# Kernel tuning notes

Measured on AMD Instinct MI355X. Metric: run time of the kernel, lower is better.

Reference implementation:

```python
import jax, jax.numpy as jnp
import numpy as np

N_NODES = 100000
N_EDGES = 1600000
IN_CH = 128
HID = 128
EPS = 1e-5


def setup_inputs() -> dict:
    key = jax.random.key(0)
    ks = jax.random.split(key, 16)
    x = jax.random.normal(ks[0], (N_NODES, IN_CH), dtype=jnp.float32)
    edge_index = jax.random.randint(ks[1], (2, N_EDGES), 0, N_NODES, dtype=jnp.int64)
    dims = [(IN_CH, HID), (HID, HID), (HID, HID // 2)]
    params = {}
    for i, (di, do) in enumerate(dims):
        params[f'w{i}'] = jax.random.normal(ks[2 + i], (di, do), dtype=jnp.float32) * (1.0 / np.sqrt(di))
        params[f'b{i}'] = jnp.zeros((do,), dtype=jnp.float32)
        params[f'g{i}'] = jnp.ones((do,), dtype=jnp.float32)
        params[f'be{i}'] = jnp.zeros((do,), dtype=jnp.float32)
    params['wc1'] = jax.random.normal(ks[8], (HID // 2, 32), dtype=jnp.float32) * (1.0 / np.sqrt(HID // 2))
    params['bc1'] = jnp.zeros((32,), dtype=jnp.float32)
    params['wc2'] = jax.random.normal(ks[9], (32, 1), dtype=jnp.float32) * (1.0 / np.sqrt(32))
    params['bc2'] = jnp.zeros((1,), dtype=jnp.float32)
    return {'x': x, 'edge_index': edge_index, **params}


def _gcn_forward(x, edge_index, w0, b0, g0, be0, w1, b1, g1, be1, w2, b2, g2, be2, wc1, bc1, wc2, bc2):
    n = x.shape[0]
    # add self-loops (GCNConv default)
    loops = jnp.arange(n, dtype=edge_index.dtype)
    src = jnp.concatenate([edge_index[0], loops])  # [E+N]
    dst = jnp.concatenate([edge_index[1], loops])
    # symmetric normalization: deg over targets (incl. self loops)
    deg = jax.ops.segment_sum(jnp.ones_like(dst, dtype=x.dtype), dst, num_segments=n)
    dis = jax.lax.rsqrt(jnp.maximum(deg, 1e-12))  # deg>=1 due to self loops
    norm = (dis[src] * dis[dst])[:, None]  # [E+N, 1]

    def layer(h, w, b, g, be):
        h = h @ w                                   # [N, d_out]
        h = jax.ops.segment_sum(h[src] * norm, dst, num_segments=n) + b
        mu = jnp.mean(h, axis=0)
        var = jnp.mean(jnp.square(h - mu), axis=0)  # biased var (torch BN)
        h = (h - mu) * jax.lax.rsqrt(var + EPS) * g + be
        return jax.nn.relu(h)                       # dropout: identity (eval)

    h = layer(x, w0, b0, g0, be0)
    h = layer(h, w1, b1, g1, be1)
    h = layer(h, w2, b2, g2, be2)
    h = jax.nn.relu(h @ wc1 + bc1)
    return (h @ wc2 + bc2)[:, 0]  # [N]


def reference(x, edge_index, w0, b0, g0, be0, w1, b1, g1, be1, w2, b2, g2, be2, wc1, bc1, wc2, bc2):
    return _gcn_forward(x, edge_index, w0, b0, g0, be0, w1, b1, g1, be1, w2, b2, g2, be2, wc1, bc1, wc2, bc2)
```

## Files before the change

### kernel.cpp

```cpp
#include <hip/hip_runtime.h>


typedef __attribute__((ext_vector_type(8))) short short8;
typedef __attribute__((ext_vector_type(4))) float f32x4;

#define BIN_SHIFT 7
#define BIN_NODES 128
#define CAPB 4096
#define CAP 64

__device__ __forceinline__ float b2f(unsigned short u) {
    return __uint_as_float(((unsigned)u) << 16);
}
__device__ __forceinline__ unsigned short f2bf(float f) {
    unsigned u = __float_as_uint(f);
    return (unsigned short)((u + 0x7fff + ((u >> 16) & 1)) >> 16);
}

__global__ __launch_bounds__(256) void part1_kernel(const int* __restrict__ eidx,
                                                    int E, int nbins, int chunk,
                                                    int* __restrict__ bin_fill,
                                                    int* __restrict__ binned) {
    __shared__ int cntS[1024];
    __shared__ int baseS[1024];
    int tid = threadIdx.x;
    for (int b = tid; b < nbins; b += 256) cntS[b] = 0;
    __syncthreads();
    int e0 = blockIdx.x * chunk;
    int e1 = min(e0 + chunk, E);
    for (int e = e0 + tid; e < e1; e += 256)
        atomicAdd(&cntS[eidx[E + e] >> BIN_SHIFT], 1);
    __syncthreads();
    for (int b = tid; b < nbins; b += 256) {
        baseS[b] = atomicAdd(&bin_fill[b], cntS[b]);
        cntS[b] = 0;
    }
    __syncthreads();
    for (int e = e0 + tid; e < e1; e += 256) {
        int d = eidx[E + e];
        int s = eidx[e];
        int b = d >> BIN_SHIFT;
        int p = baseS[b] + atomicAdd(&cntS[b], 1);
        if (p < CAPB) binned[b * CAPB + p] = (s << BIN_SHIFT) | (d & (BIN_NODES - 1));
    }
}

__global__ __launch_bounds__(256) void part2_kernel(const int* __restrict__ bin_fill,
                                                    const int* __restrict__ binned,
                                                    int N, int* __restrict__ fill,
                                                    float* __restrict__ dis,
                                                    int* __restrict__ stage) {
    __shared__ int lfill[BIN_NODES];
    int b = blockIdx.x, tid = threadIdx.x;
    if (tid < BIN_NODES) lfill[tid] = 0;
    __syncthreads();
    int cnt = min(bin_fill[b], CAPB);
    const int* seg = binned + b * CAPB;
    for (int i = tid; i < cnt; i += 256) {
        int v = seg[i];
        int dl = v & (BIN_NODES - 1);
        int p = atomicAdd(&lfill[dl], 1);
        int node = (b << BIN_SHIFT) + dl;
        if (p < CAP) stage[(node << 6) + p] = v >> BIN_SHIFT;
    }
    __syncthreads();
    if (tid < BIN_NODES) {
        int node = (b << BIN_SHIFT) + tid;
        if (node < N) {
            int c = lfill[tid];
            fill[node] = c;
            dis[node] = rsqrtf((float)c + 1.0f);
        }
    }
}

__global__ void wfrag_kernel(const float* __restrict__ w,
                             unsigned short* __restrict__ wf, int total, int C) {
    int tid = blockIdx.x * 256 + threadIdx.x;
    if (tid >= total) return;
    int j = tid & 7;
    int lane = (tid >> 3) & 63;
    int q = (tid >> 9) & 3;
    int n_tile = tid >> 11;
    int k = q * 32 + (lane >> 4) * 8 + j;
    int n = n_tile * 16 + (lane & 15);
    wf[tid] = f2bf(w[k * C + n]);
}

__device__ __forceinline__ void load8(const float* p, float4& lo, float4& hi) {
    lo = *(const float4*)p;
    hi = *(const float4*)(p + 4);
}
__device__ __forceinline__ void load8(const unsigned short* p, float4& lo, float4& hi) {
    int4 q = *(const int4*)p;
    lo = make_float4(__uint_as_float((unsigned)q.x << 16),
                     __uint_as_float((unsigned)q.x & 0xffff0000u),
                     __uint_as_float((unsigned)q.y << 16),
                     __uint_as_float((unsigned)q.y & 0xffff0000u));
    hi = make_float4(__uint_as_float((unsigned)q.z << 16),
                     __uint_as_float((unsigned)q.z & 0xffff0000u),
                     __uint_as_float((unsigned)q.w << 16),
                     __uint_as_float((unsigned)q.w & 0xffff0000u));
}

template <int C, typename InT>
__global__ __launch_bounds__(256, 5) void mfma_gemm_kernel(
    const InT* __restrict__ xin, const unsigned short* __restrict__ wf,
    const float* __restrict__ scale, const float* __restrict__ shift,
    const float* __restrict__ dis, unsigned short* __restrict__ out, int N) {
    constexpr int NT = C / 16;
    constexpr int WFRAGS = NT * 4 * 64;
    __shared__ short8 ws[WFRAGS];
    int tid = threadIdx.x;
    for (int i = tid; i < WFRAGS; i += 256) ws[i] = ((const short8*)wf)[i];

    int lane = tid & 63;
    int wave = tid >> 6;
    int m0 = blockIdx.x * 64 + wave * 16;
    int r15 = lane & 15, r4 = lane >> 4;
    f32x4 acc[NT];
#pragma unroll
    for (int t = 0; t < NT; t++) acc[t] = (f32x4){0.f, 0.f, 0.f, 0.f};
    int row0 = m0 + r15;
    int row0c = min(row0, N - 1);
    __syncthreads();

#pragma unroll
    for (int q = 0; q < 4; q++) {
        int kb = q * 32 + r4 * 8;
        float4 a0l, a0h;
        load8(xin + (size_t)row0c * 128 + kb, a0l, a0h);
        if (scale) {
            float4 scl = *(const float4*)&scale[kb];
            float4 sch = *(const float4*)&scale[kb + 4];
            float4 shl = *(const float4*)&shift[kb];
            float4 shh = *(const float4*)&shift[kb + 4];
            a0l.x = fmaxf(a0l.x * scl.x + shl.x, 0.f);
            a0l.y = fmaxf(a0l.y * scl.y + shl.y, 0.f);
            a0l.z = fmaxf(a0l.z * scl.z + shl.z, 0.f);
            a0l.w = fmaxf(a0l.w * scl.w + shl.w, 0.f);
            a0h.x = fmaxf(a0h.x * sch.x + shh.x, 0.f);
            a0h.y = fmaxf(a0h.y * sch.y + shh.y, 0.f);
            a0h.z = fmaxf(a0h.z * sch.z + shh.z, 0.f);
            a0h.w = fmaxf(a0h.w * sch.w + shh.w, 0.f);
        }
        short8 a0;
        a0[0] = (short)f2bf(a0l.x); a0[1] = (short)f2bf(a0l.y);
        a0[2] = (short)f2bf(a0l.z); a0[3] = (short)f2bf(a0l.w);
        a0[4] = (short)f2bf(a0h.x); a0[5] = (short)f2bf(a0h.y);
        a0[6] = (short)f2bf(a0h.z); a0[7] = (short)f2bf(a0h.w);
#pragma unroll
        for (int nt = 0; nt < NT; nt++) {
            short8 b = ws[(nt * 4 + q) * 64 + lane];
            acc[nt] = __builtin_amdgcn_mfma_f32_16x16x32_bf16(a0, b, acc[nt], 0, 0, 0);
        }
    }
    float d0r[4];
#pragma unroll
    for (int r = 0; r < 4; r++) {
        int rowa = m0 + r4 * 4 + r;
        d0r[r] = (rowa < N) ? dis[rowa] : 0.f;
    }
#pragma unroll
    for (int nt = 0; nt < NT; nt++) {
        int col = nt * 16 + r15;
#pragma unroll
        for (int r = 0; r < 4; r++) {
            int rowa = m0 + r4 * 4 + r;
            if (rowa < N) out[(size_t)rowa * C + col] = f2bf(acc[nt][r] * d0r[r]);
        }
    }
}

__global__ __launch_bounds__(256) void agg128_kernel(
    const unsigned short* __restrict__ h, const int* __restrict__ fill,
    const int* __restrict__ stage, const float* __restrict__ dis,
    unsigned short* __restrict__ out, int N) {
    int lane = threadIdx.x & 63;
    int node = blockIdx.x * 4 + (threadIdx.x >> 6);
    if (node >= N) return;
    float dn = dis[node];
    ushort2 sv = ((const ushort2*)(h + (size_t)node * 128))[lane];
    float2 acc = make_float2(b2f(sv.x), b2f(sv.y));
    int ne = min(fill[node], CAP);
    int pk = (lane < ne) ? stage[(node << 6) + lane] : 0;
    int j = 0;
    for (; j + 16 <= ne; j += 16) {
        ushort2 a[16];
#pragma unroll
        for (int t = 0; t < 16; t++) {
            int s = __builtin_amdgcn_readlane(pk, j + t);
            a[t] = ((const ushort2*)(h + (size_t)s * 128))[lane];
        }
#pragma unroll
        for (int t = 0; t < 16; t++) { acc.x += b2f(a[t].x); acc.y += b2f(a[t].y); }
    }
    for (; j + 8 <= ne; j += 8) {
        ushort2 a[8];
#pragma unroll
        for (int t = 0; t < 8; t++) {
            int s = __builtin_amdgcn_readlane(pk, j + t);
            a[t] = ((const ushort2*)(h + (size_t)s * 128))[lane];
        }
#pragma unroll
        for (int t = 0; t < 8; t++) { acc.x += b2f(a[t].x); acc.y += b2f(a[t].y); }
    }
    for (; j + 4 <= ne; j += 4) {
        ushort2 a[4];
#pragma unroll
        for (int t = 0; t < 4; t++) {
            int s = __builtin_amdgcn_readlane(pk, j + t);
            a[t] = ((const ushort2*)(h + (size_t)s * 128))[lane];
        }
#pragma unroll
        for (int t = 0; t < 4; t++) { acc.x += b2f(a[t].x); acc.y += b2f(a[t].y); }
    }
    for (; j < ne; j++) {
        int s = __builtin_amdgcn_readlane(pk, j);
        ushort2 a = ((const ushort2*)(h + (size_t)s * 128))[lane];
        acc.x += b2f(a.x);
        acc.y += b2f(a.y);
    }
    ((ushort2*)(out + (size_t)node * 128))[lane] =
        make_ushort2(f2bf(acc.x * dn), f2bf(acc.y * dn));
}

__global__ __launch_bounds__(256) void agg64_kernel(
    const unsigned short* __restrict__ h, const int* __restrict__ fill,
    const int* __restrict__ stage, const float* __restrict__ dis,
    unsigned short* __restrict__ out, int N) {
    int lane = threadIdx.x & 63;
    int node = blockIdx.x * 4 + (threadIdx.x >> 6);
    if (node >= N) return;
    int half = lane >> 5, ch = lane & 31;
    float dn = dis[node];
    float2 acc = make_float2(0.f, 0.f);
    if (half == 0) {
        ushort2 sv = ((const ushort2*)(h + (size_t)node * 64))[ch];
        acc.x = b2f(sv.x);
        acc.y = b2f(sv.y);
    }
    int ne = min(fill[node], CAP);
    int pk = (lane < ne) ? stage[(node << 6) + lane] : 0;
    int j = 0;
    for (; j + 16 <= ne; j += 16) {
        ushort2 a[8];
#pragma unroll
        for (int t = 0; t < 8; t++) {
            int s = __shfl(pk, j + 2 * t + half);
            a[t] = ((const ushort2*)(h + (size_t)s * 64))[ch];
        }
#pragma unroll
        for (int t = 0; t < 8; t++) { acc.x += b2f(a[t].x); acc.y += b2f(a[t].y); }
    }
    for (; j + 8 <= ne; j += 8) {
        ushort2 a[4];
#pragma unroll
        for (int t = 0; t < 4; t++) {
            int s = __shfl(pk, j + 2 * t + half);
            a[t] = ((const ushort2*)(h + (size_t)s * 64))[ch];
        }
#pragma unroll
        for (int t = 0; t < 4; t++) { acc.x += b2f(a[t].x); acc.y += b2f(a[t].y); }
    }
    for (; j < ne; j += 2) {
        int jj = j + half;
        int s = __shfl(pk, jj);
        bool v = jj < ne;
        ushort2 a = ((const ushort2*)(h + (size_t)s * 64))[ch];
        acc.x += v ? b2f(a.x) : 0.f;
        acc.y += v ? b2f(a.y) : 0.f;
    }
    acc.x += __shfl_down(acc.x, 32);
    acc.y += __shfl_down(acc.y, 32);
    if (half == 0)
        ((ushort2*)(out + (size_t)node * 64))[ch] =
            make_ushort2(f2bf(acc.x * dn), f2bf(acc.y * dn));
}

template <int C>
__global__ __launch_bounds__(256) void stats_kernel(const unsigned short* __restrict__ h,
                                                    int N, float* __restrict__ sums) {
    constexpr int R = 256 / C;
    int c = threadIdx.x % C;
    int rg = threadIdx.x / C;
    float s = 0.f, s2 = 0.f;
    for (int n = blockIdx.x * R + rg; n < N; n += gridDim.x * R) {
        float v = b2f(h[(size_t)n * C + c]);
        s += v;
        s2 += v * v;
    }
    __shared__ float red[256], red2[256];
    red[threadIdx.x] = s;
    red2[threadIdx.x] = s2;
    __syncthreads();
    if (rg == 0) {
#pragma unroll
        for (int r = 1; r < R; r++) {
            s += red[r * C + c];
            s2 += red2[r * C + c];
        }
        atomicAdd(&sums[c], s);
        atomicAdd(&sums[C + c], s2);
    }
}

template <int C>
__global__ void finalize_kernel(const float* __restrict__ sums,
                                const float* __restrict__ g,
                                const float* __restrict__ be, int N,
                                float* __restrict__ scale, float* __restrict__ shift) {
    int c = threadIdx.x;
    float inv_n = 1.0f / (float)N;
    float mean = sums[c] * inv_n;
    float var = sums[C + c] * inv_n - mean * mean;
    var = var > 0.f ? var : 0.f;
    float sc = g[c] * rsqrtf(var + 1e-5f);
    scale[c] = sc;
    shift[c] = be[c] - mean * sc;
}

__global__ __launch_bounds__(256) void head_kernel(
    const unsigned short* __restrict__ h, const float* __restrict__ scale,
    const float* __restrict__ shift, const float* __restrict__ wc1,
    const float* __restrict__ bc1, const float* __restrict__ wc2,
    const float* __restrict__ bc2, float* __restrict__ out, int N) {
    __shared__ float w1s[64 * 32];
    __shared__ float b1s[32], w2s[32], s2s[64], sh2[64];
    __shared__ float b2s;
    int tid = threadIdx.x;
    for (int i = tid; i < 64 * 32; i += 256) w1s[i] = wc1[i];
    if (tid < 32) { b1s[tid] = bc1[tid]; w2s[tid] = wc2[tid]; }
    if (tid < 64) { s2s[tid] = scale[tid]; sh2[tid] = shift[tid]; }
    if (tid == 0) b2s = bc2[0];
    __syncthreads();
    int n = blockIdx.x * 256 + tid;
    if (n >= N) return;
    float v[64];
#pragma unroll
    for (int k = 0; k < 64; k++) {
        float x = b2f(h[(size_t)n * 64 + k]) * s2s[k] + sh2[k];
        v[k] = x > 0.f ? x : 0.f;
    }
    float o = b2s;
#pragma unroll 2
    for (int j = 0; j < 32; j++) {
        float t = b1s[j];
#pragma unroll
        for (int k = 0; k < 64; k++) t += v[k] * w1s[k * 32 + j];
        t = t > 0.f ? t : 0.f;
        o += t * w2s[j];
    }
    out[n] = o;
}

extern "C" void kernel_launch(void* const* d_in, const int* in_sizes, int n_in,
                              void* d_out, int out_size, void* d_ws, size_t ws_size,
                              hipStream_t stream) {
    const float* x = (const float*)d_in[0];
    const int* eidx = (const int*)d_in[1];
    const float* w0 = (const float*)d_in[2];
    const float* g0 = (const float*)d_in[4];
    const float* be0 = (const float*)d_in[5];
    const float* w1 = (const float*)d_in[6];
    const float* g1 = (const float*)d_in[8];
    const float* be1 = (const float*)d_in[9];
    const float* w2 = (const float*)d_in[10];
    const float* g2 = (const float*)d_in[12];
    const float* be2 = (const float*)d_in[13];
    const float* wc1 = (const float*)d_in[14];
    const float* bc1 = (const float*)d_in[15];
    const float* wc2 = (const float*)d_in[16];
    const float* bc2 = (const float*)d_in[17];

    const int N = in_sizes[0] / 128;
    const int E = in_sizes[1] / 2;
    const int nbins = (N + BIN_NODES - 1) >> BIN_SHIFT;

    char* p = (char*)d_ws;
    auto alloc = [&](size_t bytes) {
        void* r = (void*)p;
        p += (bytes + 255) & ~(size_t)255;
        return r;
    };
    float* sums = (float*)alloc(3 * 256 * 4);
    int* bin_fill = (int*)alloc((size_t)nbins * 4);
    size_t zero_bytes = (size_t)(p - (char*)d_ws);
    int* fill = (int*)alloc((size_t)N * 4);
    int* binned = (int*)alloc((size_t)nbins * CAPB * 4);
    int* stage = (int*)alloc((size_t)N * CAP * 4);
    float* dis = (float*)alloc((size_t)N * 4);
    float* ss = (float*)alloc(3 * 256 * 4);
    unsigned short* hA = (unsigned short*)alloc((size_t)N * 128 * 2);
    unsigned short* hB = (unsigned short*)alloc((size_t)N * 128 * 2);
    unsigned short* wf0 = (unsigned short*)alloc(128 * 128 * 2);
    unsigned short* wf1 = (unsigned short*)alloc(128 * 128 * 2);
    unsigned short* wf2 = (unsigned short*)alloc(128 * 64 * 2);

    float* sums0 = sums, *sums1 = sums + 256, *sums2 = sums + 512;
    float* sc0 = ss, *sh0 = ss + 128;
    float* sc1 = ss + 256, *sh1 = ss + 384;
    float* sc2 = ss + 512, *sh2 = ss + 640;

    hipMemsetAsync(d_ws, 0, zero_bytes, stream);

    wfrag_kernel<<<64, 256, 0, stream>>>(w0, wf0, 128 * 128, 128);
    wfrag_kernel<<<64, 256, 0, stream>>>(w1, wf1, 128 * 128, 128);
    wfrag_kernel<<<32, 256, 0, stream>>>(w2, wf2, 128 * 64, 64);

    int p1_blocks = 256;
    int chunk = (E + p1_blocks - 1) / p1_blocks;
    part1_kernel<<<p1_blocks, 256, 0, stream>>>(eidx, E, nbins, chunk, bin_fill, binned);
    part2_kernel<<<nbins, 256, 0, stream>>>(bin_fill, binned, N, fill, dis, stage);

    int agg_grid = (N + 3) / 4;
    int gemm_grid = (N + 63) / 64;

    mfma_gemm_kernel<128, float><<<gemm_grid, 256, 0, stream>>>(x, wf0, nullptr, nullptr,
                                                                dis, hA, N);
    agg128_kernel<<<agg_grid, 256, 0, stream>>>(hA, fill, stage, dis, hB, N);
    stats_kernel<128><<<1024, 256, 0, stream>>>(hB, N, sums0);
    finalize_kernel<128><<<1, 128, 0, stream>>>(sums0, g0, be0, N, sc0, sh0);

    mfma_gemm_kernel<128, unsigned short><<<gemm_grid, 256, 0, stream>>>(
        hB, wf1, sc0, sh0, dis, hA, N);
    agg128_kernel<<<agg_grid, 256, 0, stream>>>(hA, fill, stage, dis, hB, N);
    stats_kernel<128><<<1024, 256, 0, stream>>>(hB, N, sums1);
    finalize_kernel<128><<<1, 128, 0, stream>>>(sums1, g1, be1, N, sc1, sh1);

    mfma_gemm_kernel<64, unsigned short><<<gemm_grid, 256, 0, stream>>>(
        hB, wf2, sc1, sh1, dis, hA, N);
    agg64_kernel<<<agg_grid, 256, 0, stream>>>(hA, fill, stage, dis, hB, N);
    stats_kernel<64><<<1024, 256, 0, stream>>>(hB, N, sums2);
    finalize_kernel<64><<<1, 64, 0, stream>>>(sums2, g2, be2, N, sc2, sh2);

    head_kernel<<<(N + 255) / 256, 256, 0, stream>>>(hB, sc2, sh2, wc1, bc1, wc2,
                                                     bc2, (float*)d_out, N);
}
```

Measured before the change: 518.1 us.

## Vectorize edge binning and stats loads, merge weight-fragment launches

```diff
diff --git a/kernel.cpp b/kernel.cpp
--- a/kernel.cpp
+++ b/kernel.cpp
@@ -28,20 +28,31 @@
     __syncthreads();
     int e0 = blockIdx.x * chunk;
     int e1 = min(e0 + chunk, E);
-    for (int e = e0 + tid; e < e1; e += 256)
-        atomicAdd(&cntS[eidx[E + e] >> BIN_SHIFT], 1);
+    for (int i = e0 + tid * 4; i < e1; i += 1024) {
+        int4 d4 = *(const int4*)&eidx[E + i];
+        atomicAdd(&cntS[d4.x >> BIN_SHIFT], 1);
+        atomicAdd(&cntS[d4.y >> BIN_SHIFT], 1);
+        atomicAdd(&cntS[d4.z >> BIN_SHIFT], 1);
+        atomicAdd(&cntS[d4.w >> BIN_SHIFT], 1);
+    }
     __syncthreads();
     for (int b = tid; b < nbins; b += 256) {
         baseS[b] = atomicAdd(&bin_fill[b], cntS[b]);
         cntS[b] = 0;
     }
     __syncthreads();
-    for (int e = e0 + tid; e < e1; e += 256) {
-        int d = eidx[E + e];
-        int s = eidx[e];
-        int b = d >> BIN_SHIFT;
-        int p = baseS[b] + atomicAdd(&cntS[b], 1);
-        if (p < CAPB) binned[b * CAPB + p] = (s << BIN_SHIFT) | (d & (BIN_NODES - 1));
+    for (int i = e0 + tid * 4; i < e1; i += 1024) {
+        int4 d4 = *(const int4*)&eidx[E + i];
+        int4 s4 = *(const int4*)&eidx[i];
+#pragma unroll
+        for (int k = 0; k < 4; k++) {
+            int d = (k == 0) ? d4.x : (k == 1) ? d4.y : (k == 2) ? d4.z : d4.w;
+            int s = (k == 0) ? s4.x : (k == 1) ? s4.y : (k == 2) ? s4.z : s4.w;
+            int b = d >> BIN_SHIFT;
+            int p = baseS[b] + atomicAdd(&cntS[b], 1);
+            if (p < CAPB)
+                binned[b * CAPB + p] = (s << BIN_SHIFT) | (d & (BIN_NODES - 1));
+        }
     }
 }
 
@@ -56,12 +67,17 @@
     __syncthreads();
     int cnt = min(bin_fill[b], CAPB);
     const int* seg = binned + b * CAPB;
-    for (int i = tid; i < cnt; i += 256) {
-        int v = seg[i];
-        int dl = v & (BIN_NODES - 1);
-        int p = atomicAdd(&lfill[dl], 1);
-        int node = (b << BIN_SHIFT) + dl;
-        if (p < CAP) stage[(node << 6) + p] = v >> BIN_SHIFT;
+    for (int i = tid * 4; i < cnt; i += 1024) {
+        int4 v4 = *(const int4*)&seg[i];
+#pragma unroll
+        for (int k = 0; k < 4; k++) {
+            if (i + k >= cnt) break;
+            int v = (k == 0) ? v4.x : (k == 1) ? v4.y : (k == 2) ? v4.z : v4.w;
+            int dl = v & (BIN_NODES - 1);
+            int p = atomicAdd(&lfill[dl], 1);
+            int node = (b << BIN_SHIFT) + dl;
+            if (p < CAP) stage[(node << 6) + p] = v >> BIN_SHIFT;
+        }
     }
     __syncthreads();
     if (tid < BIN_NODES) {
@@ -74,14 +90,21 @@
     }
 }
 
-__global__ void wfrag_kernel(const float* __restrict__ w,
-                             unsigned short* __restrict__ wf, int total, int C) {
+__global__ void wfrag_kernel(const float* __restrict__ w0,
+                             const float* __restrict__ w1,
+                             const float* __restrict__ w2,
+                             unsigned short* __restrict__ wf) {
     int tid = blockIdx.x * 256 + threadIdx.x;
-    if (tid >= total) return;
-    int j = tid & 7;
-    int lane = (tid >> 3) & 63;
-    int q = (tid >> 9) & 3;
-    int n_tile = tid >> 11;
+    if (tid >= 40960) return;
+    const float* w;
+    int idx, C;
+    if (tid < 16384) { w = w0; idx = tid; C = 128; }
+    else if (tid < 32768) { w = w1; idx = tid - 16384; C = 128; }
+    else { w = w2; idx = tid - 32768; C = 64; }
+    int j = idx & 7;
+    int lane = (idx >> 3) & 63;
+    int q = (idx >> 9) & 3;
+    int n_tile = idx >> 11;
     int k = q * 32 + (lane >> 4) * 8 + j;
     int n = n_tile * 16 + (lane & 15);
     wf[tid] = f2bf(w[k * C + n]);
@@ -281,27 +304,38 @@
 template <int C>
 __global__ __launch_bounds__(256) void stats_kernel(const unsigned short* __restrict__ h,
                                                     int N, float* __restrict__ sums) {
-    constexpr int R = 256 / C;
-    int c = threadIdx.x % C;
-    int rg = threadIdx.x / C;
-    float s = 0.f, s2 = 0.f;
-    for (int n = blockIdx.x * R + rg; n < N; n += gridDim.x * R) {
-        float v = b2f(h[(size_t)n * C + c]);
-        s += v;
-        s2 += v * v;
-    }
-    __shared__ float red[256], red2[256];
-    red[threadIdx.x] = s;
-    red2[threadIdx.x] = s2;
+    constexpr int CG = C / 4;
+    constexpr int RG = 256 / CG;
+    int t = threadIdx.x;
+    int cg = t % CG;
+    int rg = t / CG;
+    float s[4] = {0.f, 0.f, 0.f, 0.f}, q[4] = {0.f, 0.f, 0.f, 0.f};
+    for (int n = blockIdx.x * RG + rg; n < N; n += gridDim.x * RG) {
+        ushort4 v = *(const ushort4*)&h[(size_t)n * C + cg * 4];
+        float f0 = b2f(v.x), f1 = b2f(v.y), f2 = b2f(v.z), f3 = b2f(v.w);
+        s[0] += f0; s[1] += f1; s[2] += f2; s[3] += f3;
+        q[0] += f0 * f0; q[1] += f1 * f1; q[2] += f2 * f2; q[3] += f3 * f3;
+    }
+    __shared__ float red[RG][CG][8];
+#pragma unroll
+    for (int k = 0; k < 4; k++) {
+        red[rg][cg][k] = s[k];
+        red[rg][cg][4 + k] = q[k];
+    }
     __syncthreads();
     if (rg == 0) {
 #pragma unroll
-        for (int r = 1; r < R; r++) {
-            s += red[r * C + c];
-            s2 += red2[r * C + c];
-        }
-        atomicAdd(&sums[c], s);
-        atomicAdd(&sums[C + c], s2);
+        for (int w = 1; w < RG; w++)
+#pragma unroll
+            for (int k = 0; k < 4; k++) {
+                s[k] += red[w][cg][k];
+                q[k] += red[w][cg][4 + k];
+            }
+#pragma unroll
+        for (int k = 0; k < 4; k++) {
+            atomicAdd(&sums[cg * 4 + k], s[k]);
+            atomicAdd(&sums[C + cg * 4 + k], q[k]);
+        }
     }
 }
 
@@ -393,9 +427,10 @@
     float* ss = (float*)alloc(3 * 256 * 4);
     unsigned short* hA = (unsigned short*)alloc((size_t)N * 128 * 2);
     unsigned short* hB = (unsigned short*)alloc((size_t)N * 128 * 2);
-    unsigned short* wf0 = (unsigned short*)alloc(128 * 128 * 2);
-    unsigned short* wf1 = (unsigned short*)alloc(128 * 128 * 2);
-    unsigned short* wf2 = (unsigned short*)alloc(128 * 64 * 2);
+    unsigned short* wf = (unsigned short*)alloc(40960 * 2);
+    unsigned short* wf0 = wf;
+    unsigned short* wf1 = wf + 16384;
+    unsigned short* wf2 = wf + 32768;
 
     float* sums0 = sums, *sums1 = sums + 256, *sums2 = sums + 512;
     float* sc0 = ss, *sh0 = ss + 128;
@@ -404,12 +439,9 @@
 
     hipMemsetAsync(d_ws, 0, zero_bytes, stream);
 
-    wfrag_kernel<<<64, 256, 0, stream>>>(w0, wf0, 128 * 128, 128);
-    wfrag_kernel<<<64, 256, 0, stream>>>(w1, wf1, 128 * 128, 128);
-    wfrag_kernel<<<32, 256, 0, stream>>>(w2, wf2, 128 * 64, 64);
-
+    wfrag_kernel<<<160, 256, 0, stream>>>(w0, w1, w2, wf);
     int p1_blocks = 256;
-    int chunk = (E + p1_blocks - 1) / p1_blocks;
+    int chunk = ((E + p1_blocks - 1) / p1_blocks + 3) & ~3;
     part1_kernel<<<p1_blocks, 256, 0, stream>>>(eidx, E, nbins, chunk, bin_fill, binned);
     part2_kernel<<<nbins, 256, 0, stream>>>(bin_fill, binned, N, fill, dis, stage);
 
```

Measured after the change: 706.7 us. 1.36x slower.
